# Performance work log

Measured on AMD Instinct MI355X. Metric: run time of the kernel, lower is better.

## Reference

```python
import jax, jax.numpy as jnp
import numpy as np

N_HEADS, N_KV_HEADS, HEAD_DIM = 32, 8, 64
ROPE_BASE = 10000.0
NEG_INF = -1e30


def _rope_tables(t):
    inv_freq = 1.0 / (ROPE_BASE ** (jnp.arange(0, HEAD_DIM, 2, dtype=jnp.float32) / HEAD_DIM))
    ang = jnp.arange(t, dtype=jnp.float32)[:, None] * inv_freq[None, :]  # (t, hd/2)
    emb = jnp.concatenate([ang, ang], axis=-1)  # (t, hd)
    return jnp.cos(emb), jnp.sin(emb)


def _apply_rope(x, cos, sin):
    # x: (b, h, t, hd); cos/sin: (t, hd)
    x1, x2 = jnp.split(x, 2, axis=-1)
    rot = jnp.concatenate([-x2, x1], axis=-1)
    return x * cos[None, None] + rot * sin[None, None]


def setup_inputs() -> dict:
    key = jax.random.key(0)
    ks = jax.random.split(key, 5)
    b, t, d, kv = 4, 1024, 2048, 512
    s = 0.02
    return {
        'x': jax.random.normal(ks[0], (b, t, d), jnp.float32),
        'Wq': jax.random.normal(ks[1], (d, d), jnp.float32) * s,
        'Wk': jax.random.normal(ks[2], (d, kv), jnp.float32) * s,
        'Wv': jax.random.normal(ks[3], (d, kv), jnp.float32) * s,
        'Wo': jax.random.normal(ks[4], (d, d), jnp.float32) * s,
    }


def reference(x, Wq, Wk, Wv, Wo):
    b, t, d = x.shape
    g = N_HEADS // N_KV_HEADS
    scale = HEAD_DIM ** 0.5
    q = (x @ Wq).reshape(b, t, N_HEADS, HEAD_DIM).transpose(0, 2, 1, 3)
    k = (x @ Wk).reshape(b, t, N_KV_HEADS, HEAD_DIM).transpose(0, 2, 1, 3)
    v = (x @ Wv).reshape(b, t, N_KV_HEADS, HEAD_DIM).transpose(0, 2, 1, 3)
    cos, sin = _rope_tables(t)
    q = _apply_rope(q, cos, sin)
    k = _apply_rope(k, cos, sin)
    k = jnp.repeat(k, g, axis=1)  # GQA expand to (b, H, t, hd)
    v = jnp.repeat(v, g, axis=1)
    dot = jnp.einsum('bhqd,bhkd->bhqk', q, k)
    q_nsq = jnp.sum(q * q, axis=-1, keepdims=True)        # (b,H,t,1)
    k_nsq = jnp.sum(k * k, axis=-1, keepdims=True)        # (b,H,t,1)
    scores = (dot - 0.5 * q_nsq - 0.5 * jnp.swapaxes(k_nsq, -1, -2)) / scale
    causal = jnp.tril(jnp.ones((t, t), dtype=bool))
    scores = jnp.where(causal[None, None], scores, NEG_INF)
    attn = jax.nn.softmax(scores, axis=-1)
    y = jnp.einsum('bhqk,bhkd->bhqd', attn, v)
    y = y.transpose(0, 2, 1, 3).reshape(b, t, d)
    return y @ Wo
```

## Files before the change

### kernel.cpp

```cpp
#include <hip/hip_runtime.h>

typedef __bf16 bf16x8 __attribute__((ext_vector_type(8)));
typedef __bf16 bf16x4v __attribute__((ext_vector_type(4)));
typedef float f32x4 __attribute__((ext_vector_type(4)));

#define LDS_ASYNC16(g, l)                                            \
  __builtin_amdgcn_global_load_lds(                                  \
      (__attribute__((address_space(1))) void*)(g),                  \
      (__attribute__((address_space(3))) void*)(l), 16, 0, 0)

#define MFMA16(a, b, c) __builtin_amdgcn_mfma_f32_16x16x32_bf16(a, b, c, 0, 0, 0)

#if __has_builtin(__builtin_amdgcn_exp2f)
#define EXP2F(x) __builtin_amdgcn_exp2f(x)
#else
#define EXP2F(x) exp2f(x)
#endif

#define QSCALE 0.18033688011112042f
#define KBIAS -0.09016844005556021f

__global__ void cast_bf16(const float* __restrict__ x, __bf16* __restrict__ y,
                          int n4) {
  int i = blockIdx.x * 256 + threadIdx.x;
  if (i < n4) {
    float4 v = ((const float4*)x)[i];
    bf16x4v o;
    o[0] = (__bf16)v.x; o[1] = (__bf16)v.y; o[2] = (__bf16)v.z; o[3] = (__bf16)v.w;
    ((bf16x4v*)y)[i] = o;
  }
}

__global__ void wtrans(const float* __restrict__ src, int srcld,
                       __bf16* __restrict__ dst, int dstld) {
  __shared__ float tile[64][65];
  int k0 = blockIdx.x * 64, n0 = blockIdx.y * 64;
  int tl = threadIdx.x >> 6, c = threadIdx.x & 63;
#pragma unroll
  for (int rr = 0; rr < 16; ++rr) {
    int k = rr * 4 + tl;
    tile[k][c] = src[(size_t)(k0 + k) * srcld + n0 + c];
  }
  __syncthreads();
#pragma unroll
  for (int rr = 0; rr < 16; ++rr) {
    int n = rr * 4 + tl;
    dst[(size_t)(n0 + n) * dstld + k0 + c] = (__bf16)tile[c][n];
  }
}

template <int OUTBF16>
__global__ __launch_bounds__(256) void gemm_bt(const __bf16* __restrict__ A,
                                               const __bf16* __restrict__ B,
                                               void* __restrict__ Cout, int M,
                                               int N, int K) {
  __shared__ __bf16 As[128 * 32];
  __shared__ __bf16 Bs[128 * 32];
  int tid = threadIdx.x;
  int wave = tid >> 6, lane = tid & 63;
  int quad = lane >> 4, l16 = lane & 15;
  int wm = (wave & 1) * 64, wn = (wave >> 1) * 64;
  int tm = blockIdx.y * 128, tn = blockIdx.x * 128;

  f32x4 acc[4][4] = {};

  int srow = tid >> 2;
  int scol = (tid & 3) * 8;
  const __bf16* gA = A + (size_t)(tm + srow) * K + scol;
  const __bf16* gB = B + (size_t)(tn + srow) * K + scol;
  __bf16* lA0 = As + wave * 512;
  __bf16* lA1 = As + 2048 + wave * 512;
  __bf16* lB0 = Bs + wave * 512;
  __bf16* lB1 = Bs + 2048 + wave * 512;
  size_t stepA = (size_t)64 * K;

  for (int k0 = 0; k0 < K; k0 += 32) {
    LDS_ASYNC16(gA, lA0);
    LDS_ASYNC16(gA + stepA, lA1);
    LDS_ASYNC16(gB, lB0);
    LDS_ASYNC16(gB + stepA, lB1);
    gA += 32;
    gB += 32;
    __syncthreads();
    bf16x8 af[4], bfr[4];
#pragma unroll
    for (int mt = 0; mt < 4; ++mt)
      af[mt] = *(const bf16x8*)(As + (wm + mt * 16 + l16) * 32 + quad * 8);
#pragma unroll
    for (int nt = 0; nt < 4; ++nt)
      bfr[nt] = *(const bf16x8*)(Bs + (wn + nt * 16 + l16) * 32 + quad * 8);
#pragma unroll
    for (int mt = 0; mt < 4; ++mt)
#pragma unroll
      for (int nt = 0; nt < 4; ++nt)
        acc[mt][nt] = MFMA16(af[mt], bfr[nt], acc[mt][nt]);
    __syncthreads();
  }
  int r0 = tm + wm + quad * 4;
  int c0 = tn + wn + l16;
#pragma unroll
  for (int mt = 0; mt < 4; ++mt)
#pragma unroll
    for (int nt = 0; nt < 4; ++nt)
#pragma unroll
      for (int r = 0; r < 4; ++r) {
        size_t idx = (size_t)(r0 + mt * 16 + r) * N + (c0 + nt * 16);
        if (OUTBF16)
          ((__bf16*)Cout)[idx] = (__bf16)acc[mt][nt][r];
        else
          ((float*)Cout)[idx] = acc[mt][nt][r];
      }
}

__global__ void rope_q_kernel(const __bf16* __restrict__ qkv,
                              __bf16* __restrict__ Qr) {
  int n = blockIdx.x * 256 + threadIdx.x;
  int i = n & 31, h = (n >> 5) & 31, t = (n >> 10) & 1023, b = n >> 20;
  const __bf16* src = qkv + (size_t)(b * 1024 + t) * 3072 + h * 64;
  float x1 = (float)src[i], x2 = (float)src[i + 32];
  float ang = (float)t * expf((float)i * -0.28782313662425572f);
  float cv = cosf(ang), sv = sinf(ang);
  float o1 = (x1 * cv - x2 * sv) * QSCALE;
  float o2 = (x2 * cv + x1 * sv) * QSCALE;
  __bf16* dst = Qr + (((size_t)b * 32 + h) * 1024 + t) * 64;
  dst[i] = (__bf16)o1;
  dst[i + 32] = (__bf16)o2;
}

__global__ void rope_k_kernel(const __bf16* __restrict__ qkv,
                              __bf16* __restrict__ Kr,
                              float* __restrict__ bias2) {
  int n = blockIdx.x * 256 + threadIdx.x;
  int i = n & 31, kvh = (n >> 5) & 7, t = (n >> 8) & 1023, b = n >> 18;
  const __bf16* src = qkv + (size_t)(b * 1024 + t) * 3072 + 2048 + kvh * 64;
  float x1 = (float)src[i], x2 = (float)src[i + 32];
  float ang = (float)t * expf((float)i * -0.28782313662425572f);
  float cv = cosf(ang), sv = sinf(ang);
  float o1 = x1 * cv - x2 * sv;
  float o2 = x2 * cv + x1 * sv;
  __bf16 b1 = (__bf16)o1, b2 = (__bf16)o2;
  float f1 = (float)b1, f2 = (float)b2;
  float nrm = f1 * f1 + f2 * f2;
#pragma unroll
  for (int off = 1; off < 32; off <<= 1) nrm += __shfl_xor(nrm, off, 64);
  __bf16* dst = Kr + (((size_t)b * 8 + kvh) * 1024 + t) * 64;
  dst[i] = b1;
  dst[i + 32] = b2;
  if (i == 0) bias2[((size_t)b * 8 + kvh) * 1024 + t] = KBIAS * nrm;
}

__global__ void vtrans(const __bf16* __restrict__ qkv,
                       __bf16* __restrict__ VT) {
  __shared__ __bf16 tile[64][65];
  int tt = blockIdx.x, bkv = blockIdx.y;
  int b = bkv >> 3, kv = bkv & 7;
  int tl = threadIdx.x >> 6, d = threadIdx.x & 63;
#pragma unroll
  for (int rr = 0; rr < 16; ++rr) {
    int t_local = rr * 4 + tl;
    tile[t_local][d] =
        qkv[(size_t)(b * 1024 + tt * 64 + t_local) * 3072 + 2560 + kv * 64 + d];
  }
  __syncthreads();
#pragma unroll
  for (int rr = 0; rr < 16; ++rr) {
    int d_out = rr * 4 + tl;
    VT[((size_t)(b * 8 + kv) * 64 + d_out) * 1024 + tt * 64 + d] =
        tile[d][d_out];
  }
}

__global__ __launch_bounds__(256, 2) void attn_kernel(
    const __bf16* __restrict__ Q, const __bf16* __restrict__ Kc,
    const __bf16* __restrict__ VT, const float* __restrict__ bias2,
    __bf16* __restrict__ Y) {
  const int T = 1024;
  int h = blockIdx.x, qt = 7 - blockIdx.y, b = blockIdx.z;
  int kv = h >> 2;
  int tid = threadIdx.x;
  int wave = tid >> 6, lane = tid & 63;
  int quad = lane >> 4, l16 = lane & 15;

  __shared__ __bf16 KsA[2][8 * 128 * 8];
  __shared__ __bf16 VsA[2][16 * 64 * 8];
  __shared__ __bf16 Ps[4][8 * 32 * 8];

  const __bf16* Qb = Q + (((size_t)b * 32 + h) * T + qt * 128 + wave * 32) * 64;
  const __bf16* Kb = Kc + ((size_t)b * 8 + kv) * T * 64;
  const __bf16* Vb = VT + ((size_t)b * 8 + kv) * 64 * T;
  const float* nb = bias2 + ((size_t)b * 8 + kv) * T;
  __bf16* Pw = &Ps[wave][0];

  bf16x8 qf[2][2];
#pragma unroll
  for (int nt = 0; nt < 2; ++nt)
#pragma unroll
    for (int kd = 0; kd < 2; ++kd)
      qf[nt][kd] =
          *(const bf16x8*)(Qb + (size_t)(nt * 16 + l16) * 64 + kd * 32 + quad * 8);

  bf16x8 onesf;
#pragma unroll
  for (int u = 0; u < 8; ++u) onesf[u] = (__bf16)1.0f;

  f32x4 oacc[2][4] = {};
  f32x4 lacc[2] = {};

#define STAGE_TILE(k0_, buf_)                                                 \
  {                                                                           \
    _Pragma("unroll") for (int u = 0; u < 8; ++u) {                           \
      int t = wave * 8 + u;                                                   \
      if (t < 16) {                                                           \
        int c = t >> 1, kh = t & 1;                                           \
        LDS_ASYNC16(                                                          \
            Kb + (size_t)((k0_) + kh * 64) * 64 + c * 8 + (size_t)lane * 64,  \
            KsA[buf_] + c * 1024 + kh * 512);                                 \
      } else {                                                                \
        int c = t - 16;                                                       \
        LDS_ASYNC16(Vb + (size_t)lane * T + (k0_) + c * 8,                    \
                    VsA[buf_] + c * 512);                                     \
      }                                                                       \
    }                                                                         \
  }

  STAGE_TILE(0, 0);

  for (int j = 0; j <= qt; ++j) {
    int k0 = j * 128;
    int cur = j & 1;
    bool diag = (j == qt);

    f32x4 bv[8];
#pragma unroll
    for (int mt = 0; mt < 8; ++mt)
      bv[mt] = *(const f32x4*)(nb + k0 + mt * 16 + quad * 4);

    if (j < qt) {
      STAGE_TILE(k0 + 128, cur ^ 1);
      asm volatile("s_waitcnt vmcnt(8)" ::: "memory");
    } else {
      asm volatile("s_waitcnt vmcnt(0)" ::: "memory");
    }
    __builtin_amdgcn_s_barrier();

    const __bf16* Ksc = KsA[cur];
    const __bf16* Vsc = VsA[cur];

    f32x4 sacc[8][2];
#pragma unroll
    for (int mt = 0; mt < 8; ++mt) {
      sacc[mt][0] = bv[mt];
      sacc[mt][1] = bv[mt];
    }
#pragma unroll
    for (int kd = 0; kd < 2; ++kd)
#pragma unroll
      for (int mt = 0; mt < 8; ++mt) {
        bf16x8 kf =
            *(const bf16x8*)(Ksc + (kd * 4 + quad) * 1024 + (mt * 16 + l16) * 8);
        sacc[mt][0] = MFMA16(kf, qf[0][kd], sacc[mt][0]);
        sacc[mt][1] = MFMA16(kf, qf[1][kd], sacc[mt][1]);
      }

    if (diag) {
#pragma unroll
      for (int mt = 0; mt < 8; ++mt)
#pragma unroll
        for (int nt = 0; nt < 2; ++nt)
#pragma unroll
          for (int r = 0; r < 4; ++r) {
            int key = mt * 16 + quad * 4 + r;
            int ql = wave * 32 + nt * 16 + l16;
            if (key > ql) sacc[mt][nt][r] = -1e30f;
          }
    }

#pragma unroll
    for (int kh = 0; kh < 2; ++kh) {
#pragma unroll
      for (int mh = 0; mh < 4; ++mh) {
        int mt = 4 * kh + mh;
        int cp = 2 * mh + (quad >> 1);
        int halfo = (quad & 1) * 4;
#pragma unroll
        for (int nt = 0; nt < 2; ++nt) {
          bf16x4v pk;
#pragma unroll
          for (int r = 0; r < 4; ++r) pk[r] = (__bf16)EXP2F(sacc[mt][nt][r]);
          int qs = ((nt * 16 + l16) + 2 * cp) & 31;
          *(bf16x4v*)(Pw + cp * 256 + qs * 8 + halfo) = pk;
        }
      }
#pragma unroll
      for (int kil = 0; kil < 2; ++kil) {
        int cp = 4 * kil + quad;
        bf16x8 pf0 = *(const bf16x8*)(Pw + cp * 256 + ((l16 + 2 * cp) & 31) * 8);
        bf16x8 pf1 =
            *(const bf16x8*)(Pw + cp * 256 + ((16 + l16 + 2 * cp) & 31) * 8);
        lacc[0] = MFMA16(onesf, pf0, lacc[0]);
        lacc[1] = MFMA16(onesf, pf1, lacc[1]);
        int s = 2 * kh + kil;
#pragma unroll
        for (int dt = 0; dt < 4; ++dt) {
          bf16x8 vf = *(const bf16x8*)(Vsc + (4 * s + quad) * 512 +
                                       (dt * 16 + l16) * 8);
          oacc[0][dt] = MFMA16(vf, pf0, oacc[0][dt]);
          oacc[1][dt] = MFMA16(vf, pf1, oacc[1][dt]);
        }
      }
    }
    __builtin_amdgcn_s_barrier();
  }

#pragma unroll
  for (int nt = 0; nt < 2; ++nt) {
    float linv = 1.0f / lacc[nt][0];
    __bf16* Yr =
        Y + (((size_t)b * T + qt * 128 + wave * 32 + nt * 16 + l16) * 32 + h) * 64;
#pragma unroll
    for (int dt = 0; dt < 4; ++dt) {
      bf16x4v ov;
#pragma unroll
      for (int r = 0; r < 4; ++r) ov[r] = (__bf16)(oacc[nt][dt][r] * linv);
      *(bf16x4v*)(Yr + dt * 16 + quad * 4) = ov;
    }
  }
#undef STAGE_TILE
}

extern "C" void kernel_launch(void* const* d_in, const int* in_sizes, int n_in,
                              void* d_out, int out_size, void* d_ws,
                              size_t ws_size, hipStream_t stream) {
  const float* x = (const float*)d_in[0];
  const float* Wq = (const float*)d_in[1];
  const float* Wk = (const float*)d_in[2];
  const float* Wv = (const float*)d_in[3];
  const float* Wo = (const float*)d_in[4];
  float* out = (float*)d_out;

  char* ws = (char*)d_ws;
  __bf16* xb = (__bf16*)(ws);
  __bf16* W1T = (__bf16*)(ws + 16777216);
  __bf16* qkv = (__bf16*)(ws + 16777216 + 12582912);
  char* d4 = ws + 16777216 + 12582912 + 25165824;
  __bf16* Kr = (__bf16*)(d4);
  __bf16* VT = (__bf16*)(d4 + 4194304);
  float* bias2 = (float*)(d4 + 8388608);
  __bf16* Qr = xb;
  __bf16* WoT = W1T;
  __bf16* y = qkv;

  cast_bf16<<<8192, 256, 0, stream>>>(x, xb, 2097152);
  wtrans<<<dim3(32, 32), 256, 0, stream>>>(Wq, 2048, W1T, 2048);
  wtrans<<<dim3(32, 8), 256, 0, stream>>>(Wk, 512, W1T + 2048 * 2048, 2048);
  wtrans<<<dim3(32, 8), 256, 0, stream>>>(Wv, 512, W1T + 2560 * 2048, 2048);
  gemm_bt<1><<<dim3(24, 32), 256, 0, stream>>>(xb, W1T, qkv, 4096, 3072, 2048);
  rope_q_kernel<<<16384, 256, 0, stream>>>(qkv, Qr);
  rope_k_kernel<<<4096, 256, 0, stream>>>(qkv, Kr, bias2);
  vtrans<<<dim3(16, 32), 256, 0, stream>>>(qkv, VT);
  wtrans<<<dim3(32, 32), 256, 0, stream>>>(Wo, 2048, WoT, 2048);
  attn_kernel<<<dim3(32, 8, 4), 256, 0, stream>>>(Qr, Kr, VT, bias2, y);
  gemm_bt<0><<<dim3(16, 32), 256, 0, stream>>>(y, WoT, out, 4096, 2048, 2048);
}
```

Baseline: 317.2 us.

## Fuse RoPE, K-norm bias and V transpose into QKV GEMM epilogue; merge weight transposes

The QKV projection GEMM now applies rotary embedding, the Q scale, the K squared-norm bias and the V transpose in its epilogue. It writes Qr, Kr, VT and bias2 directly, so the bf16 qkv intermediate and the separate rope_q, rope_k and vtrans passes are gone. The four weight-transpose launches are merged into one grid. The epilogue computes sincos per element and does scattered 2-byte stores, which may slow the GEMM tail, and the workspace layout is reassigned.

```diff
diff --git a/kernel.cpp b/kernel.cpp
--- a/kernel.cpp
+++ b/kernel.cpp
@@ -19,6 +19,7 @@
 
 #define QSCALE 0.18033688011112042f
 #define KBIAS -0.09016844005556021f
+#define LN1E4_32 0.28782313662425572f
 
 __global__ void cast_bf16(const float* __restrict__ x, __bf16* __restrict__ y,
                           int n4) {
@@ -31,10 +32,26 @@
   }
 }
 
-__global__ void wtrans(const float* __restrict__ src, int srcld,
-                       __bf16* __restrict__ dst, int dstld) {
+__global__ void wtrans_all(const float* __restrict__ Wq,
+                           const float* __restrict__ Wk,
+                           const float* __restrict__ Wv,
+                           const float* __restrict__ Wo,
+                           __bf16* __restrict__ W1T, __bf16* __restrict__ WoT) {
   __shared__ float tile[64][65];
-  int k0 = blockIdx.x * 64, n0 = blockIdx.y * 64;
+  int gy = blockIdx.y;
+  const float* src;
+  int srcld, n0;
+  __bf16* dst;
+  if (gy < 32) {
+    src = Wq; srcld = 2048; dst = W1T; n0 = gy * 64;
+  } else if (gy < 40) {
+    src = Wk; srcld = 512; dst = W1T + (size_t)2048 * 2048; n0 = (gy - 32) * 64;
+  } else if (gy < 48) {
+    src = Wv; srcld = 512; dst = W1T + (size_t)2560 * 2048; n0 = (gy - 40) * 64;
+  } else {
+    src = Wo; srcld = 2048; dst = WoT; n0 = (gy - 48) * 64;
+  }
+  int k0 = blockIdx.x * 64;
   int tl = threadIdx.x >> 6, c = threadIdx.x & 63;
 #pragma unroll
   for (int rr = 0; rr < 16; ++rr) {
@@ -45,7 +62,7 @@
 #pragma unroll
   for (int rr = 0; rr < 16; ++rr) {
     int n = rr * 4 + tl;
-    dst[(size_t)(n0 + n) * dstld + k0 + c] = (__bf16)tile[c][n];
+    dst[(size_t)(n0 + n) * 2048 + k0 + c] = (__bf16)tile[c][n];
   }
 }
 
@@ -112,61 +129,124 @@
       }
 }
 
-__global__ void rope_q_kernel(const __bf16* __restrict__ qkv,
-                              __bf16* __restrict__ Qr) {
-  int n = blockIdx.x * 256 + threadIdx.x;
-  int i = n & 31, h = (n >> 5) & 31, t = (n >> 10) & 1023, b = n >> 20;
-  const __bf16* src = qkv + (size_t)(b * 1024 + t) * 3072 + h * 64;
-  float x1 = (float)src[i], x2 = (float)src[i + 32];
-  float ang = (float)t * expf((float)i * -0.28782313662425572f);
-  float cv = cosf(ang), sv = sinf(ang);
-  float o1 = (x1 * cv - x2 * sv) * QSCALE;
-  float o2 = (x2 * cv + x1 * sv) * QSCALE;
-  __bf16* dst = Qr + (((size_t)b * 32 + h) * 1024 + t) * 64;
-  dst[i] = (__bf16)o1;
-  dst[i + 32] = (__bf16)o2;
-}
-
-__global__ void rope_k_kernel(const __bf16* __restrict__ qkv,
-                              __bf16* __restrict__ Kr,
-                              float* __restrict__ bias2) {
-  int n = blockIdx.x * 256 + threadIdx.x;
-  int i = n & 31, kvh = (n >> 5) & 7, t = (n >> 8) & 1023, b = n >> 18;
-  const __bf16* src = qkv + (size_t)(b * 1024 + t) * 3072 + 2048 + kvh * 64;
-  float x1 = (float)src[i], x2 = (float)src[i + 32];
-  float ang = (float)t * expf((float)i * -0.28782313662425572f);
-  float cv = cosf(ang), sv = sinf(ang);
-  float o1 = x1 * cv - x2 * sv;
-  float o2 = x2 * cv + x1 * sv;
-  __bf16 b1 = (__bf16)o1, b2 = (__bf16)o2;
-  float f1 = (float)b1, f2 = (float)b2;
-  float nrm = f1 * f1 + f2 * f2;
-#pragma unroll
-  for (int off = 1; off < 32; off <<= 1) nrm += __shfl_xor(nrm, off, 64);
-  __bf16* dst = Kr + (((size_t)b * 8 + kvh) * 1024 + t) * 64;
-  dst[i] = b1;
-  dst[i + 32] = b2;
-  if (i == 0) bias2[((size_t)b * 8 + kvh) * 1024 + t] = KBIAS * nrm;
-}
-
-__global__ void vtrans(const __bf16* __restrict__ qkv,
-                       __bf16* __restrict__ VT) {
-  __shared__ __bf16 tile[64][65];
-  int tt = blockIdx.x, bkv = blockIdx.y;
-  int b = bkv >> 3, kv = bkv & 7;
-  int tl = threadIdx.x >> 6, d = threadIdx.x & 63;
-#pragma unroll
-  for (int rr = 0; rr < 16; ++rr) {
-    int t_local = rr * 4 + tl;
-    tile[t_local][d] =
-        qkv[(size_t)(b * 1024 + tt * 64 + t_local) * 3072 + 2560 + kv * 64 + d];
-  }
-  __syncthreads();
-#pragma unroll
-  for (int rr = 0; rr < 16; ++rr) {
-    int d_out = rr * 4 + tl;
-    VT[((size_t)(b * 8 + kv) * 64 + d_out) * 1024 + tt * 64 + d] =
-        tile[d][d_out];
+__global__ __launch_bounds__(256) void gemm_qkv(
+    const __bf16* __restrict__ A, const __bf16* __restrict__ B,
+    __bf16* __restrict__ Qr, __bf16* __restrict__ Kr, __bf16* __restrict__ VT,
+    float* __restrict__ bias2) {
+  const int K = 2048;
+  __shared__ __bf16 As[128 * 32];
+  __shared__ __bf16 Bs[128 * 32];
+  int tid = threadIdx.x;
+  int wave = tid >> 6, lane = tid & 63;
+  int quad = lane >> 4, l16 = lane & 15;
+  int wm = (wave & 1) * 64, wn = (wave >> 1) * 64;
+  int tm = blockIdx.y * 128, tn = blockIdx.x * 128;
+
+  f32x4 acc[4][4] = {};
+
+  int srow = tid >> 2;
+  int scol = (tid & 3) * 8;
+  const __bf16* gA = A + (size_t)(tm + srow) * K + scol;
+  const __bf16* gB = B + (size_t)(tn + srow) * K + scol;
+  __bf16* lA0 = As + wave * 512;
+  __bf16* lA1 = As + 2048 + wave * 512;
+  __bf16* lB0 = Bs + wave * 512;
+  __bf16* lB1 = Bs + 2048 + wave * 512;
+  size_t stepA = (size_t)64 * K;
+
+  for (int k0 = 0; k0 < K; k0 += 32) {
+    LDS_ASYNC16(gA, lA0);
+    LDS_ASYNC16(gA + stepA, lA1);
+    LDS_ASYNC16(gB, lB0);
+    LDS_ASYNC16(gB + stepA, lB1);
+    gA += 32;
+    gB += 32;
+    __syncthreads();
+    bf16x8 af[4], bfr[4];
+#pragma unroll
+    for (int mt = 0; mt < 4; ++mt)
+      af[mt] = *(const bf16x8*)(As + (wm + mt * 16 + l16) * 32 + quad * 8);
+#pragma unroll
+    for (int nt = 0; nt < 4; ++nt)
+      bfr[nt] = *(const bf16x8*)(Bs + (wn + nt * 16 + l16) * 32 + quad * 8);
+#pragma unroll
+    for (int mt = 0; mt < 4; ++mt)
+#pragma unroll
+      for (int nt = 0; nt < 4; ++nt)
+        acc[mt][nt] = MFMA16(af[mt], bfr[nt], acc[mt][nt]);
+    __syncthreads();
+  }
+
+  int r0 = tm + wm + quad * 4;
+  int c0 = tn + wn;
+
+  if (blockIdx.x < 20) {
+    bool isQ = (blockIdx.x < 16);
+    float invf0 = expf((float)l16 * -LN1E4_32);
+    float invf1 = expf((float)(l16 + 16) * -LN1E4_32);
+    int h = isQ ? (c0 >> 6) : ((c0 - 2048) >> 6);
+    __bf16* base = isQ ? Qr : Kr;
+    int nh = isQ ? 32 : 8;
+#pragma unroll
+    for (int mt = 0; mt < 4; ++mt) {
+      float nsq[4];
+#pragma unroll
+      for (int r = 0; r < 4; ++r) {
+        int row = r0 + mt * 16 + r;
+        int t = row & 1023, b = row >> 10;
+        float tf = (float)t;
+        float a0 = tf * invf0, a1 = tf * invf1;
+        float s0, c0f, s1, c1f;
+        sincosf(a0, &s0, &c0f);
+        sincosf(a1, &s1, &c1f);
+        float oa = acc[mt][0][r] * c0f - acc[mt][2][r] * s0;
+        float oc = acc[mt][2][r] * c0f + acc[mt][0][r] * s0;
+        float ob = acc[mt][1][r] * c1f - acc[mt][3][r] * s1;
+        float od = acc[mt][3][r] * c1f + acc[mt][1][r] * s1;
+        if (isQ) {
+          oa *= QSCALE; ob *= QSCALE; oc *= QSCALE; od *= QSCALE;
+        }
+        __bf16 ba = (__bf16)oa, bb = (__bf16)ob, bc = (__bf16)oc,
+               bd = (__bf16)od;
+        __bf16* dst = base + (((size_t)b * nh + h) * 1024 + t) * 64;
+        dst[l16] = ba;
+        dst[16 + l16] = bb;
+        dst[32 + l16] = bc;
+        dst[48 + l16] = bd;
+        float fa = (float)ba, fb = (float)bb, fc = (float)bc, fd = (float)bd;
+        nsq[r] = fa * fa + fb * fb + fc * fc + fd * fd;
+      }
+      if (!isQ) {
+#pragma unroll
+        for (int r = 0; r < 4; ++r) {
+          float nl = nsq[r];
+          nl += __shfl_xor(nl, 1);
+          nl += __shfl_xor(nl, 2);
+          nl += __shfl_xor(nl, 4);
+          nl += __shfl_xor(nl, 8);
+          if (l16 == 0) {
+            int row = r0 + mt * 16 + r;
+            int t = row & 1023, b = row >> 10;
+            bias2[((size_t)b * 8 + h) * 1024 + t] = KBIAS * nl;
+          }
+        }
+      }
+    }
+  } else {
+    int kvh = (c0 - 2560) >> 6;
+#pragma unroll
+    for (int mt = 0; mt < 4; ++mt) {
+      int rowb = r0 + mt * 16;
+      int t = rowb & 1023, b = rowb >> 10;
+#pragma unroll
+      for (int nt = 0; nt < 4; ++nt) {
+        int d = nt * 16 + l16;
+        bf16x4v ov;
+#pragma unroll
+        for (int r = 0; r < 4; ++r) ov[r] = (__bf16)acc[mt][nt][r];
+        *(bf16x4v*)(VT + ((size_t)(b * 8 + kvh) * 64 + d) * 1024 + t) = ov;
+      }
+    }
   }
 }
 
@@ -341,24 +421,17 @@
   char* ws = (char*)d_ws;
   __bf16* xb = (__bf16*)(ws);
   __bf16* W1T = (__bf16*)(ws + 16777216);
-  __bf16* qkv = (__bf16*)(ws + 16777216 + 12582912);
-  char* d4 = ws + 16777216 + 12582912 + 25165824;
-  __bf16* Kr = (__bf16*)(d4);
-  __bf16* VT = (__bf16*)(d4 + 4194304);
-  float* bias2 = (float*)(d4 + 8388608);
-  __bf16* Qr = xb;
-  __bf16* WoT = W1T;
-  __bf16* y = qkv;
+  __bf16* WoT = (__bf16*)(ws + 16777216 + 12582912);
+  char* d4 = ws + 16777216 + 12582912 + 8388608;
+  __bf16* Qr = (__bf16*)(d4);
+  __bf16* Kr = (__bf16*)(d4 + 16777216);
+  __bf16* VT = (__bf16*)(d4 + 16777216 + 4194304);
+  float* bias2 = (float*)(d4 + 16777216 + 8388608);
+  __bf16* y = xb;
 
   cast_bf16<<<8192, 256, 0, stream>>>(x, xb, 2097152);
-  wtrans<<<dim3(32, 32), 256, 0, stream>>>(Wq, 2048, W1T, 2048);
-  wtrans<<<dim3(32, 8), 256, 0, stream>>>(Wk, 512, W1T + 2048 * 2048, 2048);
-  wtrans<<<dim3(32, 8), 256, 0, stream>>>(Wv, 512, W1T + 2560 * 2048, 2048);
-  gemm_bt<1><<<dim3(24, 32), 256, 0, stream>>>(xb, W1T, qkv, 4096, 3072, 2048);
-  rope_q_kernel<<<16384, 256, 0, stream>>>(qkv, Qr);
-  rope_k_kernel<<<4096, 256, 0, stream>>>(qkv, Kr, bias2);
-  vtrans<<<dim3(16, 32), 256, 0, stream>>>(qkv, VT);
-  wtrans<<<dim3(32, 32), 256, 0, stream>>>(Wo, 2048, WoT, 2048);
+  wtrans_all<<<dim3(32, 80), 256, 0, stream>>>(Wq, Wk, Wv, Wo, W1T, WoT);
+  gemm_qkv<<<dim3(24, 32), 256, 0, stream>>>(xb, W1T, Qr, Kr, VT, bias2);
   attn_kernel<<<dim3(32, 8, 4), 256, 0, stream>>>(Qr, Kr, VT, bias2, y);
   gemm_bt<0><<<dim3(16, 32), 256, 0, stream>>>(y, WoT, out, 4096, 2048, 2048);
 }
```

Result: faster. 286.4 us (-9.7%).
